# Kernel optimization log

Measured on AMD Instinct MI355X. Metric: run time of the kernel, lower is better.

The kernel has to match this reference:

```python
import jax, jax.numpy as jnp
import numpy as np

NUM_CLASSES = 41
EPS = 1e-12


def nearest_resize(lab, h, w):
    # torch F.interpolate(mode='nearest'): src_idx = floor(dst_idx * in / out)
    Hl, Wl = lab.shape[1], lab.shape[2]
    ih = (jnp.arange(h) * Hl) // h
    iw = (jnp.arange(w) * Wl) // w
    return lab[:, ih][:, :, iw]


def segment_mean(feats, lab_small, base):
    # feats [b,c,h,w], lab_small [b,h,w] int, base [b,L,c] (values for absent labels)
    b, c, h, w = feats.shape
    L = NUM_CLASSES
    lab = lab_small.reshape(b, h * w)
    ids = (jnp.arange(b, dtype=lab.dtype)[:, None] * L + lab).reshape(-1)  # [b*h*w]
    x = feats.reshape(b, c, h * w).transpose(0, 2, 1).reshape(-1, c)       # [b*h*w, c]
    sums = jax.ops.segment_sum(x, ids, num_segments=b * L).reshape(b, L, c)
    cnts = jax.ops.segment_sum(jnp.ones((b * h * w,), feats.dtype), ids,
                               num_segments=b * L).reshape(b, L, 1)
    mean = sums / jnp.maximum(cnts, 1.0)
    return jnp.where(cnts > 0, mean, base)


def ra_gate(feats, lab_small, base, w1, w2):
    # RA.forward: segment-mean queue -> L2 normalize over class dim -> sum -> 1x1 convs -> sigmoid
    att = segment_mean(feats, lab_small, base)                      # [b,L,c]
    nrm = jnp.sqrt(jnp.sum(att * att, axis=1, keepdims=True))       # over classes (dim=1)
    att = att / jnp.maximum(nrm, EPS)
    s = jnp.sum(att, axis=1)                                        # [b,c]
    h1 = jax.nn.relu(jnp.einsum('bc,oc->bo', s, w1))                # conv1 1x1, no bias
    g = jax.nn.sigmoid(jnp.einsum('bo,co->bc', h1, w2))             # conv2 1x1, no bias
    return g[:, :, None, None]                                      # [b,c,1,1]


def conv3x3(x, w):
    return jax.lax.conv_general_dilated(
        x, w, window_strides=(1, 1), padding=((1, 1), (1, 1)),
        dimension_numbers=('NCHW', 'OIHW', 'NCHW'))


def setup_inputs() -> dict:
    key = jax.random.key(0)
    ks = jax.random.split(key, 10)
    B, C, H, W = 8, 128, 128, 128
    return {
        'r': jax.random.normal(ks[0], (B, C, H, W), jnp.float32),
        'd': jax.random.normal(ks[1], (B, C, H, W), jnp.float32),
        'label': jax.random.randint(ks[2], (B, 4 * H, 4 * W), 0, NUM_CLASSES, jnp.int32),
        'conv_w': jax.random.normal(ks[3], (C, 2 * C, 3, 3), jnp.float32) * 0.05,
        'f_w1': jax.random.normal(ks[4], (C // 16, C), jnp.float32) * 0.05,
        'f_w2': jax.random.normal(ks[5], (C, C // 16), jnp.float32) * 0.05,
        'd_w1': jax.random.normal(ks[6], (C // 16, C), jnp.float32) * 0.05,
        'd_w2': jax.random.normal(ks[7], (C, C // 16), jnp.float32) * 0.05,
        'seg_base_f': jax.random.normal(ks[8], (B, NUM_CLASSES, C), jnp.float32),
        'seg_base_d': jax.random.normal(ks[9], (B, NUM_CLASSES, C), jnp.float32),
    }


def reference(r, d, label, conv_w, f_w1, f_w2, d_w1, d_w2, seg_base_f, seg_base_d):
    b, c, h, w = r.shape
    add = r + d
    mul = r * jax.nn.sigmoid(d)
    fuse = conv3x3(jnp.concatenate([add, mul], axis=1), conv_w)
    lab_small = nearest_resize(label, h, w)
    d_ra = d * ra_gate(d, lab_small, seg_base_d, d_w1, d_w2)
    fuse_ra = fuse * ra_gate(fuse, lab_small, seg_base_f, f_w1, f_w2)
    return fuse_ra + d_ra
```

## Files before the change

kernel.cpp:

```cpp
#include <hip/hip_runtime.h>
#include <math.h>

typedef unsigned short u16;
typedef unsigned char u8;
typedef unsigned int u32;
typedef __bf16 bf16x8 __attribute__((ext_vector_type(8)));
typedef float f32x4 __attribute__((ext_vector_type(4)));

#define NL 41
#define HW 16384

#define NHWC_OFF   0
#define WA_OFF     67108864
#define LAB8_OFF   67698688
#define GHIST_OFF  67829760
#define SUMS_OFF   67831808
#define GATES_OFF  68167680

__device__ __forceinline__ u16 f2bf(float f) {
    u32 u = __builtin_bit_cast(u32, f);
    u = (u + 0x7FFFu + ((u >> 16) & 1u)) >> 16;
    return (u16)u;
}

__device__ __forceinline__ void glds16(const void* g, void* l) {
    __builtin_amdgcn_global_load_lds(
        (const __attribute__((address_space(1))) void*)g,
        (__attribute__((address_space(3))) void*)l, 16, 0, 0);
}

__global__ __launch_bounds__(64)
void k_wpack(const float* __restrict__ w, u16* __restrict__ wa, int* __restrict__ ghist)
{
    const int bid = (int)blockIdx.x;
    const int l = (int)threadIdx.x;
    if (bid == 0) {
        for (int i = l; i < 8 * NL; i += 64) ghist[i] = 0;
    }
    const int kt = bid >> 3, ct = bid & 7;
    const int chunk = kt / 9, tap = kt - chunk * 9;
    const int co = ct * 16 + (l & 15);
    const int cin0 = chunk * 32 + (l >> 4) * 8;
    u16 tmp[8];
#pragma unroll
    for (int j = 0; j < 8; ++j)
        tmp[j] = f2bf(w[((size_t)co * 256 + cin0 + j) * 9 + tap]);
    *(f32x4*)&wa[((size_t)bid * 64 + l) * 8] = *(f32x4*)tmp;
}

__global__ __launch_bounds__(256, 4)
void k_prep(const float* __restrict__ r, const float* __restrict__ d,
            const int* __restrict__ label, u16* __restrict__ nhwc,
            u8* __restrict__ lab8, int* __restrict__ ghist)
{
    __shared__ u16 s[64 * 256];
    __shared__ int hist[NL];
    const int bid = (int)blockIdx.x;
    const int b = bid >> 8;
    const int px0 = (bid & 255) * 64;
    const int tid = (int)threadIdx.x;
    const int c = tid & 127;
    const int half = tid >> 7;

    if (tid < NL) hist[tid] = 0;
    if (tid < 64) {
        int px = px0 + tid;
        int yy = px >> 7, xx = px & 127;
        int lab = label[(size_t)b * 512 * 512 + (yy * 4) * 512 + xx * 4];
        lab8[b * HW + px] = (u8)lab;
        atomicAdd(&hist[lab], 1);
    }

    const float* rp = r + ((size_t)(b * 128 + c)) * HW + px0 + half * 32;
    const float* dp = d + ((size_t)(b * 128 + c)) * HW + px0 + half * 32;
#pragma unroll
    for (int j = 0; j < 8; ++j) {
        float4 rv = *(const float4*)(rp + j * 4);
        float4 dv = *(const float4*)(dp + j * 4);
        float ra[4] = {rv.x, rv.y, rv.z, rv.w};
        float da[4] = {dv.x, dv.y, dv.z, dv.w};
#pragma unroll
        for (int i = 0; i < 4; ++i) {
            int px = half * 32 + j * 4 + i;
            s[px * 256 + c] = f2bf(ra[i] + da[i]);
            s[px * 256 + 128 + c] = f2bf(ra[i] / (1.f + __expf(-da[i])));
        }
    }
    __syncthreads();
    const f32x4* sf = (const f32x4*)s;
    f32x4* dst = (f32x4*)nhwc + ((size_t)b * HW + px0) * 32;
#pragma unroll
    for (int k = 0; k < 8; ++k) {
        int fi = k * 256 + tid;
        dst[fi] = sf[fi];
    }
    if (tid < NL && hist[tid] > 0) atomicAdd(&ghist[b * NL + tid], hist[tid]);
}

__global__ __launch_bounds__(256, 2)
void k_conv(const u16* __restrict__ nhwc, const u16* __restrict__ wa,
            float* __restrict__ out)
{
    __shared__ u16 s_in[2 * 2080 * 8];
    const int tid = (int)threadIdx.x;
    const int bid = (int)blockIdx.x;
    const int b = bid & 7;
    const int y0 = (bid >> 3) * 2;
    const int l = tid & 63;
    const int wv = tid >> 6;
    const int wr = wv & 1;
    const int wc = wv >> 1;
    const int l15 = l & 15;
    const int l16 = l >> 4;

    {
        f32x4 zz = {0.f, 0.f, 0.f, 0.f};
        for (int i = tid; i < 4160; i += 256) ((f32x4*)s_in)[i] = zz;
    }

    int goff[9];
#pragma unroll
    for (int it = 0; it < 9; ++it) {
        int s = it * 256 + tid;
        int row = s / 520;
        int rem = s - row * 520;
        int xslot = rem >> 2;
        int ci8 = rem & 3;
        int gy = y0 - 1 + row;
        int gx = xslot - 1;
        bool valid = (s < 2080) && ((unsigned)gy < 128u) && ((unsigned)gx < 128u);
        goff[it] = valid ? (((gy << 7) | gx) * 256 + ci8 * 8) * 2 : -1;
    }

    f32x4 acc[4][8];
#pragma unroll
    for (int i = 0; i < 4; ++i)
#pragma unroll
        for (int j = 0; j < 8; ++j) {
            f32x4 zz = {0.f, 0.f, 0.f, 0.f};
            acc[i][j] = zz;
        }

    const char* src_b = (const char*)(nhwc + (size_t)b * HW * 256);
    const int lane_base = (tid & 192) * 16;
    const f32x4* wa4 = (const f32x4*)wa;

    __syncthreads();
#pragma unroll
    for (int it = 0; it < 9; ++it)
        if (goff[it] >= 0)
            glds16(src_b + goff[it], (char*)s_in + it * 4096 + lane_base);

#pragma unroll 1
    for (int chunk = 0; chunk < 8; ++chunk) {
        __syncthreads();

        f32x4 a0[4], a1[4];
        {
            int kt8 = chunk * 72;
#pragma unroll
            for (int i = 0; i < 4; ++i) a0[i] = wa4[(kt8 + wc * 4 + i) * 64 + l];
#pragma unroll
            for (int i = 0; i < 4; ++i) a1[i] = wa4[(kt8 + 8 + wc * 4 + i) * 64 + l];
        }
        if (chunk < 7) {
            char* dstb = (char*)s_in + ((chunk + 1) & 1) * 33280 + lane_base;
#pragma unroll
            for (int it = 0; it < 9; ++it)
                if (goff[it] >= 0)
                    glds16(src_b + goff[it] + (chunk + 1) * 64, dstb + it * 4096);
        }

        const char* bufp = (const char*)s_in + (chunk & 1) * 33280;
#pragma unroll
        for (int tap = 0; tap < 9; ++tap) {
            f32x4 aC[4];
#pragma unroll
            for (int i = 0; i < 4; ++i) aC[i] = a0[i];
#pragma unroll
            for (int i = 0; i < 4; ++i) a0[i] = a1[i];
            if (tap + 2 < 9) {
                int kt8 = chunk * 72 + (tap + 2) * 8;
#pragma unroll
                for (int i = 0; i < 4; ++i)
                    a1[i] = wa4[(kt8 + wc * 4 + i) * 64 + l];
            }
            const int rowi = wr + tap / 3;
            const int dxo = tap % 3;
            f32x4 bf[8];
#pragma unroll
            for (int p = 0; p < 8; ++p) {
                int e = (rowi * 130 + p * 16 + l15 + dxo) * 64 + l16 * 16;
                bf[p] = *(const f32x4*)(bufp + e);
            }
#pragma unroll
            for (int ct = 0; ct < 4; ++ct) {
                bf16x8 av = __builtin_bit_cast(bf16x8, aC[ct]);
#pragma unroll
                for (int p = 0; p < 8; ++p)
                    acc[ct][p] = __builtin_amdgcn_mfma_f32_16x16x32_bf16(
                        av, __builtin_bit_cast(bf16x8, bf[p]), acc[ct][p], 0, 0, 0);
            }
        }
    }

    const int y = y0 + wr;
    float* outb = out + (size_t)b * 128 * HW + (size_t)y * 128;
#pragma unroll
    for (int ct = 0; ct < 4; ++ct)
#pragma unroll
        for (int p = 0; p < 8; ++p) {
            int x = p * 16 + l15;
#pragma unroll
            for (int rr = 0; rr < 4; ++rr) {
                int co = wc * 64 + ct * 16 + l16 * 4 + rr;
                outb[(size_t)co * HW + x] = acc[ct][p][rr];
            }
        }
}

__global__ __launch_bounds__(256, 3)
void k_seg(const float* __restrict__ fuse, const float* __restrict__ d,
           const u8* __restrict__ lab8, float* __restrict__ sums)
{
    __shared__ float bins[NL][256];
    const int bid = (int)blockIdx.x;
    const int feat = bid & 1;
    const int c = (bid >> 1) & 127;
    const int b = bid >> 8;
    const int tid = (int)threadIdx.x;

    for (int i = tid; i < NL * 256; i += 256) ((float*)bins)[i] = 0.f;
    __syncthreads();

    const float* src = (feat ? d : fuse) + ((size_t)(b * 128 + c)) * HW;
    const u8* lp = lab8 + b * HW;

#pragma unroll 4
    for (int k = 0; k < 16; ++k) {
        int i = k * 256 + tid;
        float4 v = ((const float4*)src)[i];
        uchar4 lv = ((const uchar4*)lp)[i];
        bins[lv.x][tid] += v.x;
        bins[lv.y][tid] += v.y;
        bins[lv.z][tid] += v.z;
        bins[lv.w][tid] += v.w;
    }
    __syncthreads();

    for (int stride = 128; stride >= 1; stride >>= 1) {
        for (int idx = tid; idx < NL * stride; idx += 256) {
            int l = idx / stride;
            int cc = idx - l * stride;
            bins[l][cc] += bins[l][cc + stride];
        }
        __syncthreads();
    }
    if (tid < NL)
        sums[(size_t)((b * 2 + feat) * NL + tid) * 128 + c] = bins[tid][0];
}

__global__ __launch_bounds__(128)
void k_gates(const float* __restrict__ sums, const int* __restrict__ ghist,
             const float* __restrict__ base_f, const float* __restrict__ base_d,
             const float* __restrict__ f_w1, const float* __restrict__ f_w2,
             const float* __restrict__ d_w1, const float* __restrict__ d_w2,
             float* __restrict__ gates)
{
    __shared__ float sv[128];
    __shared__ float h1[8];
    const int b = (int)blockIdx.x >> 1;
    const int feat = (int)blockIdx.x & 1;
    const int c = (int)threadIdx.x;

    const float* base = feat ? base_d : base_f;
    float suma = 0.f, sumsq = 0.f;
    for (int lc = 0; lc < NL; ++lc) {
        float s = sums[(size_t)((b * 2 + feat) * NL + lc) * 128 + c];
        int cnt = ghist[b * NL + lc];
        float att = (cnt > 0) ? (s / (float)cnt) : base[(b * NL + lc) * 128 + c];
        suma += att;
        sumsq += att * att;
    }
    sv[c] = suma / fmaxf(sqrtf(sumsq), 1e-12f);
    __syncthreads();

    const float* w1 = feat ? d_w1 : f_w1;
    const float* w2 = feat ? d_w2 : f_w2;
    if (c < 8) {
        float h = 0.f;
        for (int k = 0; k < 128; ++k) h += w1[c * 128 + k] * sv[k];
        h1[c] = fmaxf(h, 0.f);
    }
    __syncthreads();

    float gv = 0.f;
#pragma unroll
    for (int o = 0; o < 8; ++o) gv += w2[c * 8 + o] * h1[o];
    gates[feat * 1024 + b * 128 + c] = 1.f / (1.f + expf(-gv));
}

__global__ __launch_bounds__(256)
void k_final(const float* __restrict__ d, const float* __restrict__ gates,
             float* out)
{
    size_t t4 = (size_t)blockIdx.x * 256 + threadIdx.x;
    size_t basei = t4 * 4;
    int bc = (int)(basei >> 14);
    float gf = gates[bc];
    float gd = gates[1024 + bc];
    float4 f = *(const float4*)(out + basei);
    float4 dv = *(const float4*)(d + basei);
    float4 o;
    o.x = f.x * gf + dv.x * gd;
    o.y = f.y * gf + dv.y * gd;
    o.z = f.z * gf + dv.z * gd;
    o.w = f.w * gf + dv.w * gd;
    *(float4*)(out + basei) = o;
}

extern "C" void kernel_launch(void* const* d_in, const int* in_sizes, int n_in,
                              void* d_out, int out_size, void* d_ws, size_t ws_size,
                              hipStream_t stream)
{
    (void)in_sizes; (void)n_in; (void)out_size; (void)ws_size;
    const float* r      = (const float*)d_in[0];
    const float* d      = (const float*)d_in[1];
    const int*   label  = (const int*)d_in[2];
    const float* conv_w = (const float*)d_in[3];
    const float* f_w1   = (const float*)d_in[4];
    const float* f_w2   = (const float*)d_in[5];
    const float* d_w1   = (const float*)d_in[6];
    const float* d_w2   = (const float*)d_in[7];
    const float* base_f = (const float*)d_in[8];
    const float* base_d = (const float*)d_in[9];
    float* out = (float*)d_out;

    char* ws = (char*)d_ws;
    u16* nhwc    = (u16*)(ws + NHWC_OFF);
    u16* wa      = (u16*)(ws + WA_OFF);
    u8*  lab8    = (u8*)(ws + LAB8_OFF);
    int* ghist   = (int*)(ws + GHIST_OFF);
    float* sums  = (float*)(ws + SUMS_OFF);
    float* gates = (float*)(ws + GATES_OFF);

    hipLaunchKernelGGL(k_wpack, dim3(576), dim3(64), 0, stream, conv_w, wa, ghist);
    hipLaunchKernelGGL(k_prep, dim3(2048), dim3(256), 0, stream, r, d, label,
                       nhwc, lab8, ghist);
    hipLaunchKernelGGL(k_conv, dim3(512), dim3(256), 0, stream, nhwc, wa, out);
    hipLaunchKernelGGL(k_seg, dim3(2048), dim3(256), 0, stream, out, d, lab8, sums);
    hipLaunchKernelGGL(k_gates, dim3(16), dim3(128), 0, stream, sums, ghist,
                       base_f, base_d, f_w1, f_w2, d_w1, d_w2, gates);
    hipLaunchKernelGGL(k_final, dim3(16384), dim3(256), 0, stream, d, gates, out);
}
```

Before: 361.5 us.

## Fuse segment sums into prep and conv epilogues with fixed-point atomics

Removes the separate segment-sum kernel. The d-feature per-label sums are now accumulated in shared memory inside the prep kernel, and the fuse-feature sums are binned from the conv accumulators in the conv epilogue. Partial sums are merged globally with 64-bit fixed-point integer atomics so the result does not depend on ordering, and k_gates reads them back from that format. This avoids re-reading the full fuse and d tensors, at the cost of heavier shared-memory atomics in the conv epilogue, larger prep blocks with lower occupancy, and fixed-point quantization of the sums.

Result: slower. 429.9 us (+18.9%).

```diff
diff --git a/kernel.cpp b/kernel.cpp
--- a/kernel.cpp
+++ b/kernel.cpp
@@ -4,6 +4,7 @@
 typedef unsigned short u16;
 typedef unsigned char u8;
 typedef unsigned int u32;
+typedef unsigned long long u64;
 typedef __bf16 bf16x8 __attribute__((ext_vector_type(8)));
 typedef float f32x4 __attribute__((ext_vector_type(4)));
 
@@ -14,8 +15,8 @@
 #define WA_OFF     67108864
 #define LAB8_OFF   67698688
 #define GHIST_OFF  67829760
-#define SUMS_OFF   67831808
-#define GATES_OFF  68167680
+#define ISUM_OFF   67831808
+#define GATES_OFF  68503552
 
 __device__ __forceinline__ u16 f2bf(float f) {
     u32 u = __builtin_bit_cast(u32, f);
@@ -29,13 +30,21 @@
         (__attribute__((address_space(3))) void*)l, 16, 0, 0);
 }
 
+#define ISUM_SCALE 4294967296.f
+#define ISUM_INV   2.3283064365386963e-10f
+
 __global__ __launch_bounds__(64)
-void k_wpack(const float* __restrict__ w, u16* __restrict__ wa, int* __restrict__ ghist)
+void k_wpack(const float* __restrict__ w, u16* __restrict__ wa,
+             int* __restrict__ ghist, u64* __restrict__ isum)
 {
     const int bid = (int)blockIdx.x;
     const int l = (int)threadIdx.x;
     if (bid == 0) {
         for (int i = l; i < 8 * NL; i += 64) ghist[i] = 0;
+    }
+    if (bid < 64) {
+        u64* p = isum + bid * 1312;
+        for (int i = l; i < 1312; i += 64) p[i] = 0ull;
     }
     const int kt = bid >> 3, ct = bid & 7;
     const int chunk = kt / 9, tap = kt - chunk * 9;
@@ -48,60 +57,88 @@
     *(f32x4*)&wa[((size_t)bid * 64 + l) * 8] = *(f32x4*)tmp;
 }
 
-__global__ __launch_bounds__(256, 4)
+__global__ __launch_bounds__(256, 2)
 void k_prep(const float* __restrict__ r, const float* __restrict__ d,
             const int* __restrict__ label, u16* __restrict__ nhwc,
-            u8* __restrict__ lab8, int* __restrict__ ghist)
+            u8* __restrict__ lab8, int* __restrict__ ghist,
+            u64* __restrict__ isum_d)
 {
     __shared__ u16 s[64 * 256];
+    __shared__ float binsd[NL * 256];
     __shared__ int hist[NL];
+    __shared__ u8 s_lab[256];
     const int bid = (int)blockIdx.x;
-    const int b = bid >> 8;
-    const int px0 = (bid & 255) * 64;
+    const int b = bid >> 6;
+    const int px0 = (bid & 63) * 256;
     const int tid = (int)threadIdx.x;
     const int c = tid & 127;
     const int half = tid >> 7;
 
     if (tid < NL) hist[tid] = 0;
-    if (tid < 64) {
+    for (int i = tid; i < NL * 64; i += 256) ((f32x4*)binsd)[i] = f32x4{0,0,0,0};
+    __syncthreads();
+
+    {
         int px = px0 + tid;
         int yy = px >> 7, xx = px & 127;
         int lab = label[(size_t)b * 512 * 512 + (yy * 4) * 512 + xx * 4];
         lab8[b * HW + px] = (u8)lab;
+        s_lab[tid] = (u8)lab;
         atomicAdd(&hist[lab], 1);
     }
-
-    const float* rp = r + ((size_t)(b * 128 + c)) * HW + px0 + half * 32;
-    const float* dp = d + ((size_t)(b * 128 + c)) * HW + px0 + half * 32;
-#pragma unroll
-    for (int j = 0; j < 8; ++j) {
-        float4 rv = *(const float4*)(rp + j * 4);
-        float4 dv = *(const float4*)(dp + j * 4);
-        float ra[4] = {rv.x, rv.y, rv.z, rv.w};
-        float da[4] = {dv.x, dv.y, dv.z, dv.w};
-#pragma unroll
-        for (int i = 0; i < 4; ++i) {
-            int px = half * 32 + j * 4 + i;
-            s[px * 256 + c] = f2bf(ra[i] + da[i]);
-            s[px * 256 + 128 + c] = f2bf(ra[i] / (1.f + __expf(-da[i])));
-        }
-    }
-    __syncthreads();
-    const f32x4* sf = (const f32x4*)s;
-    f32x4* dst = (f32x4*)nhwc + ((size_t)b * HW + px0) * 32;
-#pragma unroll
-    for (int k = 0; k < 8; ++k) {
-        int fi = k * 256 + tid;
-        dst[fi] = sf[fi];
+    __syncthreads();
+
+    for (int t = 0; t < 4; ++t) {
+        const int pxb = px0 + t * 64 + half * 32;
+        const float* rp = r + ((size_t)(b * 128 + c)) * HW + pxb;
+        const float* dp = d + ((size_t)(b * 128 + c)) * HW + pxb;
+        const u8* lp = &s_lab[t * 64 + half * 32];
+        uint4 lw0 = *(const uint4*)lp;
+        uint4 lw1 = *(const uint4*)(lp + 16);
+        u32 lwords[8] = {lw0.x, lw0.y, lw0.z, lw0.w, lw1.x, lw1.y, lw1.z, lw1.w};
+#pragma unroll
+        for (int j = 0; j < 8; ++j) {
+            float4 rv = *(const float4*)(rp + j * 4);
+            float4 dv = *(const float4*)(dp + j * 4);
+            float ra[4] = {rv.x, rv.y, rv.z, rv.w};
+            float da[4] = {dv.x, dv.y, dv.z, dv.w};
+#pragma unroll
+            for (int i = 0; i < 4; ++i) {
+                int pxl = half * 32 + j * 4 + i;
+                s[pxl * 256 + c] = f2bf(ra[i] + da[i]);
+                s[pxl * 256 + 128 + c] = f2bf(ra[i] / (1.f + __expf(-da[i])));
+                int lab = (int)((lwords[j] >> (i * 8)) & 0xffu);
+                binsd[lab * 256 + tid] += da[i];
+            }
+        }
+        __syncthreads();
+        const f32x4* sf = (const f32x4*)s;
+        f32x4* dst = (f32x4*)nhwc + ((size_t)b * HW + px0 + t * 64) * 32;
+#pragma unroll
+        for (int k = 0; k < 8; ++k) {
+            int fi = k * 256 + tid;
+            dst[fi] = sf[fi];
+        }
+        __syncthreads();
+    }
+    for (int i = tid; i < NL * 128; i += 256) {
+        int lab = i >> 7, cc = i & 127;
+        float v = binsd[lab * 256 + cc] + binsd[lab * 256 + 128 + cc];
+        if (v != 0.f) {
+            long long q = (long long)(v * ISUM_SCALE);
+            atomicAdd(&isum_d[(b * NL + lab) * 128 + cc], (u64)q);
+        }
     }
     if (tid < NL && hist[tid] > 0) atomicAdd(&ghist[b * NL + tid], hist[tid]);
 }
 
 __global__ __launch_bounds__(256, 2)
 void k_conv(const u16* __restrict__ nhwc, const u16* __restrict__ wa,
-            float* __restrict__ out)
+            const u8* __restrict__ lab8, float* __restrict__ out,
+            u64* __restrict__ isum_f)
 {
     __shared__ u16 s_in[2 * 2080 * 8];
+    __shared__ u8 s_lab[256];
     const int tid = (int)threadIdx.x;
     const int bid = (int)blockIdx.x;
     const int b = bid & 7;
@@ -117,6 +154,7 @@
         f32x4 zz = {0.f, 0.f, 0.f, 0.f};
         for (int i = tid; i < 4160; i += 256) ((f32x4*)s_in)[i] = zz;
     }
+    s_lab[tid] = lab8[b * HW + y0 * 128 + tid];
 
     int goff[9];
 #pragma unroll
@@ -217,51 +255,34 @@
                 outb[(size_t)co * HW + x] = acc[ct][p][rr];
             }
         }
-}
-
-__global__ __launch_bounds__(256, 3)
-void k_seg(const float* __restrict__ fuse, const float* __restrict__ d,
-           const u8* __restrict__ lab8, float* __restrict__ sums)
-{
-    __shared__ float bins[NL][256];
-    const int bid = (int)blockIdx.x;
-    const int feat = bid & 1;
-    const int c = (bid >> 1) & 127;
-    const int b = bid >> 8;
-    const int tid = (int)threadIdx.x;
-
-    for (int i = tid; i < NL * 256; i += 256) ((float*)bins)[i] = 0.f;
-    __syncthreads();
-
-    const float* src = (feat ? d : fuse) + ((size_t)(b * 128 + c)) * HW;
-    const u8* lp = lab8 + b * HW;
-
-#pragma unroll 4
-    for (int k = 0; k < 16; ++k) {
-        int i = k * 256 + tid;
-        float4 v = ((const float4*)src)[i];
-        uchar4 lv = ((const uchar4*)lp)[i];
-        bins[lv.x][tid] += v.x;
-        bins[lv.y][tid] += v.y;
-        bins[lv.z][tid] += v.z;
-        bins[lv.w][tid] += v.w;
-    }
-    __syncthreads();
-
-    for (int stride = 128; stride >= 1; stride >>= 1) {
-        for (int idx = tid; idx < NL * stride; idx += 256) {
-            int l = idx / stride;
-            int cc = idx - l * stride;
-            bins[l][cc] += bins[l][cc + stride];
-        }
-        __syncthreads();
-    }
-    if (tid < NL)
-        sums[(size_t)((b * 2 + feat) * NL + tid) * 128 + c] = bins[tid][0];
+
+    __syncthreads();
+    float* binsf = (float*)s_in;
+    for (int i = tid; i < NL * 133; i += 256) binsf[i] = 0.f;
+    __syncthreads();
+#pragma unroll
+    for (int ct = 0; ct < 4; ++ct)
+#pragma unroll
+        for (int p = 0; p < 8; ++p) {
+            int lab = (int)s_lab[wr * 128 + p * 16 + l15];
+            float* bp = &binsf[lab * 133 + wc * 64 + ct * 16 + l16 * 4];
+#pragma unroll
+            for (int rr = 0; rr < 4; ++rr)
+                atomicAdd(bp + rr, acc[ct][p][rr]);
+        }
+    __syncthreads();
+    for (int i = tid; i < NL * 128; i += 256) {
+        int lab = i >> 7, cc = i & 127;
+        float v = binsf[lab * 133 + cc];
+        if (v != 0.f) {
+            long long q = (long long)(v * ISUM_SCALE);
+            atomicAdd(&isum_f[(b * NL + lab) * 128 + cc], (u64)q);
+        }
+    }
 }
 
 __global__ __launch_bounds__(128)
-void k_gates(const float* __restrict__ sums, const int* __restrict__ ghist,
+void k_gates(const u64* __restrict__ isum, const int* __restrict__ ghist,
              const float* __restrict__ base_f, const float* __restrict__ base_d,
              const float* __restrict__ f_w1, const float* __restrict__ f_w2,
              const float* __restrict__ d_w1, const float* __restrict__ d_w2,
@@ -276,7 +297,8 @@
     const float* base = feat ? base_d : base_f;
     float suma = 0.f, sumsq = 0.f;
     for (int lc = 0; lc < NL; ++lc) {
-        float s = sums[(size_t)((b * 2 + feat) * NL + lc) * 128 + c];
+        long long q = (long long)isum[((size_t)(feat * 8 + b) * NL + lc) * 128 + c];
+        float s = (float)q * ISUM_INV;
         int cnt = ghist[b * NL + lc];
         float att = (cnt > 0) ? (s / (float)cnt) : base[(b * NL + lc) * 128 + c];
         suma += att;
@@ -341,15 +363,18 @@
     u16* wa      = (u16*)(ws + WA_OFF);
     u8*  lab8    = (u8*)(ws + LAB8_OFF);
     int* ghist   = (int*)(ws + GHIST_OFF);
-    float* sums  = (float*)(ws + SUMS_OFF);
+    u64* isum    = (u64*)(ws + ISUM_OFF);
+    u64* isum_f  = isum;
+    u64* isum_d  = isum + 8 * NL * 128;
     float* gates = (float*)(ws + GATES_OFF);
 
-    hipLaunchKernelGGL(k_wpack, dim3(576), dim3(64), 0, stream, conv_w, wa, ghist);
-    hipLaunchKernelGGL(k_prep, dim3(2048), dim3(256), 0, stream, r, d, label,
-                       nhwc, lab8, ghist);
-    hipLaunchKernelGGL(k_conv, dim3(512), dim3(256), 0, stream, nhwc, wa, out);
-    hipLaunchKernelGGL(k_seg, dim3(2048), dim3(256), 0, stream, out, d, lab8, sums);
-    hipLaunchKernelGGL(k_gates, dim3(16), dim3(128), 0, stream, sums, ghist,
+    hipLaunchKernelGGL(k_wpack, dim3(576), dim3(64), 0, stream, conv_w, wa,
+                       ghist, isum);
+    hipLaunchKernelGGL(k_prep, dim3(512), dim3(256), 0, stream, r, d, label,
+                       nhwc, lab8, ghist, isum_d);
+    hipLaunchKernelGGL(k_conv, dim3(512), dim3(256), 0, stream, nhwc, wa,
+                       lab8, out, isum_f);
+    hipLaunchKernelGGL(k_gates, dim3(16), dim3(128), 0, stream, isum, ghist,
                        base_f, base_d, f_w1, f_w2, d_w1, d_w2, gates);
     hipLaunchKernelGGL(k_final, dim3(16384), dim3(256), 0, stream, d, gates, out);
 }
```
